# Kernel tuning notes

Hardware: AMD Instinct MI355X
Metric: run time of the kernel (lower is better)

## Reference

```python
import jax, jax.numpy as jnp
import numpy as np

N_NODES = 100000
IN_CH = 128
HID = 16
N_EDGES = 3200000


def setup_inputs() -> dict:
    key = jax.random.key(0)
    k1, k2, k3, k4 = jax.random.split(key, 4)
    x = jax.random.normal(k1, (N_NODES, IN_CH), dtype=jnp.float32)
    edge_index = jax.random.randint(k2, (2, N_EDGES), 0, N_NODES, dtype=jnp.int64)
    s1 = 1.0 / np.sqrt(IN_CH)
    s2 = 1.0 / np.sqrt(HID)
    W1 = jax.random.uniform(k3, (IN_CH, HID), dtype=jnp.float32, minval=-s1, maxval=s1)
    b1 = jnp.zeros((HID,), dtype=jnp.float32)
    W2 = jax.random.uniform(k4, (HID, HID), dtype=jnp.float32, minval=-s2, maxval=s2)
    b2 = jnp.zeros((HID,), dtype=jnp.float32)
    return {"x": x, "edge_index": edge_index, "W1": W1, "b1": b1, "W2": W2, "b2": b2}


def _gcn_layer(h, W, b, row, col, norm, n_nodes):
    # GCNConv: transform first (small hidden dim), then normalized sum aggregation
    h = h @ W  # [N, out]
    msg = h[row] * norm[:, None]  # gather over edges incl. self-loops
    out = jax.ops.segment_sum(msg, col, num_segments=n_nodes)
    return out + b


def reference(x, edge_index, W1, b1, W2, b2):
    n = x.shape[0]
    row, col = edge_index[0], edge_index[1]
    # add self-loops (PyG GCNConv default)
    loop = jnp.arange(n, dtype=edge_index.dtype)
    row_l = jnp.concatenate([row, loop])
    col_l = jnp.concatenate([col, loop])
    # symmetric normalization D^-1/2 (A+I) D^-1/2 (degree from target index)
    deg = jax.ops.segment_sum(jnp.ones_like(col_l, dtype=x.dtype), col_l, num_segments=n)
    dinv = jnp.where(deg > 0, jax.lax.rsqrt(deg), 0.0)
    norm = dinv[row_l] * dinv[col_l]

    h = _gcn_layer(x, W1, b1, row_l, col_l, norm, n)
    h = jax.nn.relu(h)  # dropout is identity at eval
    h = _gcn_layer(h, W2, b2, row_l, col_l, norm, n)

    # fused per-edge dot-product link score + sigmoid (original edges only)
    scores = jnp.sum(h[row] * h[col], axis=-1)
    return jax.nn.sigmoid(scores)
```

## Files before the change

### kernel.cpp

```cpp
#include <hip/hip_runtime.h>
#include <hip/hip_bf16.h>
#include <hip/hip_fp16.h>
#include <math.h>


#define BSH 9
#define BSZ 512
#define CAPB 32768
#define MAXCH 3200
#define MAXCHUNKS 1024

__global__ __launch_bounds__(512) void pSort(
    const int* __restrict__ row, const int* __restrict__ col,
    int* __restrict__ gcur, unsigned int* __restrict__ ebuf,
    int E, int CH, int NBUK) {
    __shared__ unsigned int se[MAXCH];
    __shared__ unsigned short pk[MAXCH];
    __shared__ int lhist[256], lbase[256], lcur[256], gbase[256];
    const int t = threadIdx.x, b = blockIdx.x;
    if (t < 256) lhist[t] = 0;
    __syncthreads();
    const int s = b * CH, e = min(E, s + CH);
    const int cnt = e - s;
    const int n4 = cnt >> 2;
    const int4* c4 = (const int4*)(col + s);
    const int4* r4 = (const int4*)(row + s);
    for (int i = t; i < n4; i += 512) {
        int4 c = c4[i];
        atomicAdd(&lhist[c.x >> BSH], 1);
        atomicAdd(&lhist[c.y >> BSH], 1);
        atomicAdd(&lhist[c.z >> BSH], 1);
        atomicAdd(&lhist[c.w >> BSH], 1);
    }
    for (int i = (n4 << 2) + t; i < cnt; i += 512) atomicAdd(&lhist[col[s + i] >> BSH], 1);
    __syncthreads();
    {
        int own = (t < 256) ? lhist[t] : 0;
        if (t < 256) lcur[t] = own;
        __syncthreads();
        for (int d = 1; d < 256; d <<= 1) {
            int add = (t < 256 && t >= d) ? lcur[t - d] : 0;
            __syncthreads();
            if (t < 256) lcur[t] += add;
            __syncthreads();
        }
        if (t < 256) {
            lbase[t] = lcur[t] - own;
            lcur[t] = lcur[t] - own;
        }
        __syncthreads();
        if (t < NBUK) {
            int base = atomicAdd(&gcur[t], lhist[t]);
            gbase[t] = t * CAPB + base - lbase[t];
        }
    }
    __syncthreads();
    for (int i = t; i < n4; i += 512) {
        int4 c = c4[i];
        int4 r = r4[i];
        int k0 = c.x >> BSH, p0 = atomicAdd(&lcur[k0], 1);
        se[p0] = ((unsigned int)(c.x & (BSZ - 1)) << 17) | (unsigned int)r.x; pk[p0] = (unsigned short)k0;
        int k1 = c.y >> BSH, p1 = atomicAdd(&lcur[k1], 1);
        se[p1] = ((unsigned int)(c.y & (BSZ - 1)) << 17) | (unsigned int)r.y; pk[p1] = (unsigned short)k1;
        int k2 = c.z >> BSH, p2 = atomicAdd(&lcur[k2], 1);
        se[p2] = ((unsigned int)(c.z & (BSZ - 1)) << 17) | (unsigned int)r.z; pk[p2] = (unsigned short)k2;
        int k3 = c.w >> BSH, p3 = atomicAdd(&lcur[k3], 1);
        se[p3] = ((unsigned int)(c.w & (BSZ - 1)) << 17) | (unsigned int)r.w; pk[p3] = (unsigned short)k3;
    }
    for (int i = (n4 << 2) + t; i < cnt; i += 512) {
        int c = col[s + i], r = row[s + i];
        int k = c >> BSH, p = atomicAdd(&lcur[k], 1);
        se[p] = ((unsigned int)(c & (BSZ - 1)) << 17) | (unsigned int)r; pk[p] = (unsigned short)k;
    }
    __syncthreads();
    for (int i = t; i < cnt; i += 512) {
        int k = pk[i];
        ebuf[gbase[k] + i] = se[i];
    }
}

__global__ __launch_bounds__(1024) void pS2G(
    const unsigned int* __restrict__ ebuf, const int* __restrict__ gcur,
    const float* __restrict__ x, const float* __restrict__ W1,
    unsigned int* __restrict__ ebuf2, float* __restrict__ dinv,
    int* __restrict__ start, __half* __restrict__ ts, int N) {
    __shared__ int h[BSZ], sc[BSZ], cur[BSZ];
    __shared__ float wsT[16 * 132];
    const int t = threadIdx.x, k = blockIdx.x;
    if (t < BSZ) h[t] = 0;
    for (int idx = t; idx < 2048; idx += 1024) {
        int kk = idx >> 4, c = idx & 15;
        wsT[c * 132 + kk] = W1[idx];
    }
    __syncthreads();
    const int s = k * CAPB, e = s + gcur[k];
    for (int i = s + t; i < e; i += 1024) atomicAdd(&h[ebuf[i] >> 17], 1);
    __syncthreads();
    if (t < BSZ) sc[t] = h[t];
    __syncthreads();
    for (int d = 1; d < BSZ; d <<= 1) {
        int add = (t < BSZ && t >= d) ? sc[t - d] : 0;
        __syncthreads();
        if (t < BSZ) sc[t] += add;
        __syncthreads();
    }
    if (t < BSZ) {
        cur[t] = sc[t] - h[t];
        const int v = (k << BSH) + t;
        if (v < N) {
            dinv[v] = rsqrtf((float)h[t] + 1.0f);
            start[v] = s + cur[t];
        }
    }
    __syncthreads();
    for (int i = s + t; i < e; i += 1024) {
        unsigned int w = ebuf[i];
        int p = atomicAdd(&cur[w >> 17], 1);
        ebuf2[s + p] = w;
    }
    const int u = t >> 1, half = t & 1;
    const int v = (k << BSH) + u;
    if (v >= N) return;
    const float dv = rsqrtf((float)h[u] + 1.0f);
    const float4* xr = (const float4*)(x + (size_t)v * 128) + half * 16;
    float acc[16];
    #pragma unroll
    for (int c = 0; c < 16; ++c) acc[c] = 0.f;
    const int kbase = half * 16;
    #pragma unroll 8
    for (int k4 = 0; k4 < 16; ++k4) {
        float4 a = xr[k4];
        #pragma unroll
        for (int c = 0; c < 16; ++c) {
            const float4 w = *(const float4*)&wsT[c * 132 + (kbase + k4) * 4];
            acc[c] = fmaf(a.x, w.x, fmaf(a.y, w.y, fmaf(a.z, w.z, fmaf(a.w, w.w, acc[c]))));
        }
    }
    #pragma unroll
    for (int c = 0; c < 16; ++c) acc[c] += __shfl_xor(acc[c], 1);
    union { __half h8[8]; uint4 u4; } o;
    #pragma unroll
    for (int c = 0; c < 8; ++c) o.h8[c] = __float2half(acc[half * 8 + c] * dv);
    ((uint4*)(ts + (size_t)v * 16))[half] = o.u4;
}

__global__ __launch_bounds__(256) void pGat1(
    const unsigned int* __restrict__ ebuf2, const int* __restrict__ start,
    const int* __restrict__ gcur,
    const __half2* __restrict__ tsv, const float* __restrict__ dinv,
    const float* __restrict__ b1, const float* __restrict__ W2,
    __half2* __restrict__ ts2v, int N) {
    __shared__ float w2s[256];
    const int tid = threadIdx.x;
    w2s[tid] = W2[tid];
    __syncthreads();
    const int l = tid & 7;
    const int v = blockIdx.x * 32 + (tid >> 3);
    if (v >= N) return;
    const int s = start[v];
    const int k = v >> BSH;
    const bool lastv = (((v + 1) & (BSZ - 1)) == 0) || (v + 1 >= N);
    const int e = lastv ? (k * CAPB + gcur[k]) : start[v + 1];
    float sx = 0.f, sy = 0.f;
    int i = s;
    for (; i + 8 <= e; i += 8) {
        unsigned int w0 = ebuf2[i],     w1 = ebuf2[i + 1];
        unsigned int w2 = ebuf2[i + 2], w3 = ebuf2[i + 3];
        unsigned int w4 = ebuf2[i + 4], w5 = ebuf2[i + 5];
        unsigned int w6 = ebuf2[i + 6], w7 = ebuf2[i + 7];
        float2 f0 = __half22float2(tsv[(size_t)(w0 & 0x1FFFF) * 8 + l]);
        float2 f1 = __half22float2(tsv[(size_t)(w1 & 0x1FFFF) * 8 + l]);
        float2 f2 = __half22float2(tsv[(size_t)(w2 & 0x1FFFF) * 8 + l]);
        float2 f3 = __half22float2(tsv[(size_t)(w3 & 0x1FFFF) * 8 + l]);
        float2 f4 = __half22float2(tsv[(size_t)(w4 & 0x1FFFF) * 8 + l]);
        float2 f5 = __half22float2(tsv[(size_t)(w5 & 0x1FFFF) * 8 + l]);
        float2 f6 = __half22float2(tsv[(size_t)(w6 & 0x1FFFF) * 8 + l]);
        float2 f7 = __half22float2(tsv[(size_t)(w7 & 0x1FFFF) * 8 + l]);
        sx += ((f0.x + f1.x) + (f2.x + f3.x)) + ((f4.x + f5.x) + (f6.x + f7.x));
        sy += ((f0.y + f1.y) + (f2.y + f3.y)) + ((f4.y + f5.y) + (f6.y + f7.y));
    }
    for (; i + 4 <= e; i += 4) {
        unsigned int w0 = ebuf2[i],     w1 = ebuf2[i + 1];
        unsigned int w2 = ebuf2[i + 2], w3 = ebuf2[i + 3];
        float2 f0 = __half22float2(tsv[(size_t)(w0 & 0x1FFFF) * 8 + l]);
        float2 f1 = __half22float2(tsv[(size_t)(w1 & 0x1FFFF) * 8 + l]);
        float2 f2 = __half22float2(tsv[(size_t)(w2 & 0x1FFFF) * 8 + l]);
        float2 f3 = __half22float2(tsv[(size_t)(w3 & 0x1FFFF) * 8 + l]);
        sx += (f0.x + f1.x) + (f2.x + f3.x);
        sy += (f0.y + f1.y) + (f2.y + f3.y);
    }
    for (; i < e; ++i) {
        unsigned int w = ebuf2[i];
        float2 f = __half22float2(tsv[(size_t)(w & 0x1FFFF) * 8 + l]);
        sx += f.x; sy += f.y;
    }
    const float dv = dinv[v];
    float2 sf = __half22float2(tsv[(size_t)v * 8 + l]);
    float hx = fmaxf(dv * (sx + sf.x) + b1[2 * l],     0.f);
    float hy = fmaxf(dv * (sy + sf.y) + b1[2 * l + 1], 0.f);
    float ox = 0.f, oy = 0.f;
    #pragma unroll
    for (int j = 0; j < 8; ++j) {
        float ax = __shfl(hx, j, 8);
        float ay = __shfl(hy, j, 8);
        ox = fmaf(ax, w2s[(2 * j) * 16 + 2 * l],     fmaf(ay, w2s[(2 * j + 1) * 16 + 2 * l],     ox));
        oy = fmaf(ax, w2s[(2 * j) * 16 + 2 * l + 1], fmaf(ay, w2s[(2 * j + 1) * 16 + 2 * l + 1], oy));
    }
    ts2v[(size_t)v * 8 + l] = __halves2half2(__float2half(dv * ox), __float2half(dv * oy));
}

__global__ __launch_bounds__(256) void pGat2(
    const unsigned int* __restrict__ ebuf2, const int* __restrict__ start,
    const int* __restrict__ gcur,
    const __half2* __restrict__ tsv, const float* __restrict__ dinv,
    const float* __restrict__ b2, __half2* __restrict__ h2v, int N) {
    const int tid = threadIdx.x;
    const int l = tid & 7;
    const int v = blockIdx.x * 32 + (tid >> 3);
    if (v >= N) return;
    const int s = start[v];
    const int k = v >> BSH;
    const bool lastv = (((v + 1) & (BSZ - 1)) == 0) || (v + 1 >= N);
    const int e = lastv ? (k * CAPB + gcur[k]) : start[v + 1];
    float sx = 0.f, sy = 0.f;
    int i = s;
    for (; i + 8 <= e; i += 8) {
        unsigned int w0 = ebuf2[i],     w1 = ebuf2[i + 1];
        unsigned int w2 = ebuf2[i + 2], w3 = ebuf2[i + 3];
        unsigned int w4 = ebuf2[i + 4], w5 = ebuf2[i + 5];
        unsigned int w6 = ebuf2[i + 6], w7 = ebuf2[i + 7];
        float2 f0 = __half22float2(tsv[(size_t)(w0 & 0x1FFFF) * 8 + l]);
        float2 f1 = __half22float2(tsv[(size_t)(w1 & 0x1FFFF) * 8 + l]);
        float2 f2 = __half22float2(tsv[(size_t)(w2 & 0x1FFFF) * 8 + l]);
        float2 f3 = __half22float2(tsv[(size_t)(w3 & 0x1FFFF) * 8 + l]);
        float2 f4 = __half22float2(tsv[(size_t)(w4 & 0x1FFFF) * 8 + l]);
        float2 f5 = __half22float2(tsv[(size_t)(w5 & 0x1FFFF) * 8 + l]);
        float2 f6 = __half22float2(tsv[(size_t)(w6 & 0x1FFFF) * 8 + l]);
        float2 f7 = __half22float2(tsv[(size_t)(w7 & 0x1FFFF) * 8 + l]);
        sx += ((f0.x + f1.x) + (f2.x + f3.x)) + ((f4.x + f5.x) + (f6.x + f7.x));
        sy += ((f0.y + f1.y) + (f2.y + f3.y)) + ((f4.y + f5.y) + (f6.y + f7.y));
    }
    for (; i + 4 <= e; i += 4) {
        unsigned int w0 = ebuf2[i],     w1 = ebuf2[i + 1];
        unsigned int w2 = ebuf2[i + 2], w3 = ebuf2[i + 3];
        float2 f0 = __half22float2(tsv[(size_t)(w0 & 0x1FFFF) * 8 + l]);
        float2 f1 = __half22float2(tsv[(size_t)(w1 & 0x1FFFF) * 8 + l]);
        float2 f2 = __half22float2(tsv[(size_t)(w2 & 0x1FFFF) * 8 + l]);
        float2 f3 = __half22float2(tsv[(size_t)(w3 & 0x1FFFF) * 8 + l]);
        sx += (f0.x + f1.x) + (f2.x + f3.x);
        sy += (f0.y + f1.y) + (f2.y + f3.y);
    }
    for (; i < e; ++i) {
        unsigned int w = ebuf2[i];
        float2 f = __half22float2(tsv[(size_t)(w & 0x1FFFF) * 8 + l]);
        sx += f.x; sy += f.y;
    }
    float2 sf = __half22float2(tsv[(size_t)v * 8 + l]);
    const float dv = dinv[v];
    h2v[(size_t)v * 8 + l] = __halves2half2(
        __float2half(dv * (sx + sf.x) + b2[2 * l]),
        __float2half(dv * (sy + sf.y) + b2[2 * l + 1]));
}

__global__ void k_score(const int* __restrict__ row, const int* __restrict__ col,
                        const __half* __restrict__ h2h, float* __restrict__ out, int E) {
    int e = blockIdx.x * 256 + threadIdx.x;
    if (e < E) {
        union { uint4 u[2]; __half2 h[8]; } a, b;
        const uint4* pa = (const uint4*)(h2h + (size_t)row[e] * 16);
        const uint4* pb = (const uint4*)(h2h + (size_t)col[e] * 16);
        a.u[0] = pa[0]; a.u[1] = pa[1];
        b.u[0] = pb[0]; b.u[1] = pb[1];
        float d = 0.f;
        #pragma unroll
        for (int i = 0; i < 8; ++i) {
            float2 fa = __half22float2(a.h[i]);
            float2 fb = __half22float2(b.h[i]);
            d = fmaf(fa.x, fb.x, fmaf(fa.y, fb.y, d));
        }
        out[e] = 1.0f / (1.0f + __expf(-d));
    }
}

__global__ void k_countf(const int* __restrict__ col, float* __restrict__ deg, int E) {
    int e = blockIdx.x * 256 + threadIdx.x;
    if (e < E) atomicAdd(&deg[col[e]], 1.0f);
}
__global__ void k_dinvf(float* __restrict__ dinv, int N) {
    int v = blockIdx.x * 256 + threadIdx.x;
    if (v < N) dinv[v] = rsqrtf(dinv[v] + 1.0f);
}
__global__ __launch_bounds__(256) void k_gemm1f(
    const float* __restrict__ x, const float* __restrict__ W1,
    const float* __restrict__ dinv, float* __restrict__ ts, int N) {
    __shared__ float wsT[16 * 132];
    const int tid = threadIdx.x;
    for (int idx = tid; idx < 2048; idx += 256) {
        int k = idx >> 4, c = idx & 15;
        wsT[c * 132 + k] = W1[idx];
    }
    __syncthreads();
    const int n = blockIdx.x * 256 + tid;
    if (n >= N) return;
    const float4* xr = (const float4*)(x + (size_t)n * 128);
    float acc[16];
    #pragma unroll
    for (int c = 0; c < 16; ++c) acc[c] = 0.f;
    for (int k4 = 0; k4 < 32; ++k4) {
        float4 a = xr[k4];
        #pragma unroll
        for (int c = 0; c < 16; ++c) {
            const float4 w = *(const float4*)&wsT[c * 132 + k4 * 4];
            acc[c] = fmaf(a.x, w.x, fmaf(a.y, w.y, fmaf(a.z, w.z, fmaf(a.w, w.w, acc[c]))));
        }
    }
    float dv = dinv[n];
    float4* o = (float4*)(ts + (size_t)n * 16);
    #pragma unroll
    for (int q = 0; q < 4; ++q)
        o[q] = make_float4(acc[4*q] * dv, acc[4*q+1] * dv, acc[4*q+2] * dv, acc[4*q+3] * dv);
}
__global__ void k_scatter(const int* __restrict__ row, const int* __restrict__ col,
                          const float* __restrict__ ts, float* __restrict__ acc, int E) {
    int g = blockIdx.x * 256 + threadIdx.x;
    int e = g >> 4, c = g & 15;
    if (e < E) atomicAdd(&acc[(size_t)col[e] * 16 + c], ts[(size_t)row[e] * 16 + c]);
}
__global__ void k_finalize(float* __restrict__ acc, const float* __restrict__ ts,
                           const float* __restrict__ dinv, const float* __restrict__ b,
                           int N, int relu) {
    int g = blockIdx.x * 256 + threadIdx.x;
    int v = g >> 4, c = g & 15;
    if (v < N) {
        float h = dinv[v] * (acc[g] + ts[g]) + b[c];
        if (relu) h = fmaxf(h, 0.f);
        acc[g] = h;
    }
}
__global__ __launch_bounds__(256) void k_gemm2f(
    const float* __restrict__ h1, const float* __restrict__ W2,
    const float* __restrict__ dinv, float* __restrict__ ts2, int N) {
    __shared__ float hs[16 * 17];
    __shared__ float ws2[256];
    const int tid = threadIdx.x;
    const int base = blockIdx.x * 16;
    if (tid < 64) ((float4*)ws2)[tid] = ((const float4*)W2)[tid];
    if (tid >= 64 && tid < 128) {
        int t2 = tid - 64;
        float4 v4 = ((const float4*)(h1 + (size_t)base * 16))[t2];
        float* d = &hs[(t2 >> 2) * 17 + (t2 & 3) * 4];
        d[0] = v4.x; d[1] = v4.y; d[2] = v4.z; d[3] = v4.w;
    }
    __syncthreads();
    const int r = tid >> 4, c = tid & 15;
    float a = 0.f;
    #pragma unroll
    for (int kk = 0; kk < 16; ++kk) a = fmaf(hs[r * 17 + kk], ws2[kk * 16 + c], a);
    ts2[(size_t)(base + r) * 16 + c] = a * dinv[base + r];
}
__global__ void k_scoref(const int* __restrict__ row, const int* __restrict__ col,
                         const float* __restrict__ h2, float* __restrict__ out, int E) {
    int e = blockIdx.x * 256 + threadIdx.x;
    if (e < E) {
        const float4* a = (const float4*)(h2 + (size_t)row[e] * 16);
        const float4* b = (const float4*)(h2 + (size_t)col[e] * 16);
        float d = 0.f;
        #pragma unroll
        for (int i = 0; i < 4; ++i) {
            float4 u = a[i], v = b[i];
            d += u.x * v.x + u.y * v.y + u.z * v.z + u.w * v.w;
        }
        out[e] = 1.0f / (1.0f + __expf(-d));
    }
}

extern "C" void kernel_launch(void* const* d_in, const int* in_sizes, int n_in,
                              void* d_out, int out_size, void* d_ws, size_t ws_size,
                              hipStream_t stream) {
    const float* x  = (const float*)d_in[0];
    const int*   ei = (const int*)d_in[1];
    const float* W1 = (const float*)d_in[2];
    const float* b1 = (const float*)d_in[3];
    const float* W2 = (const float*)d_in[4];
    const float* b2 = (const float*)d_in[5];

    const int N = in_sizes[0] / 128;
    const int E = in_sizes[1] / 2;
    const int* row = ei;
    const int* col = ei + E;
    float* out = (float*)d_out;

    const int NBUK = (N + BSZ - 1) / BSZ;
    const int CN = (E + MAXCH - 1) / MAXCH;
    const int CH = MAXCH;

    char* ws = (char*)d_ws;
    size_t off = 0;
    auto alloc = [&](size_t bytes) { void* p = ws + off; off += (bytes + 255) & ~(size_t)255; return p; };
    float*  dinv  = (float*)alloc((size_t)N * 4);
    __half* ts1h  = (__half*)alloc((size_t)N * 32);
    __half* ts2h  = (__half*)alloc((size_t)N * 32);
    int*    start = (int*)alloc((size_t)(N + 1) * 4);
    int*    gcur  = (int*)alloc((size_t)NBUK * 4);
    unsigned int* ebuf  = (unsigned int*)alloc((size_t)NBUK * CAPB * 4);
    unsigned int* ebuf2 = (unsigned int*)alloc((size_t)NBUK * CAPB * 4);
    const size_t need = off;

    if (N <= 131072 && NBUK <= 256 && CN <= MAXCHUNKS &&
        (size_t)E * 2 <= (size_t)NBUK * CAPB && ws_size >= need) {
        hipMemsetAsync(gcur, 0, (size_t)NBUK * 4, stream);
        pSort<<<CN, 512, 0, stream>>>(row, col, gcur, ebuf, E, CH, NBUK);
        pS2G<<<NBUK, 1024, 0, stream>>>(ebuf, gcur, x, W1, ebuf2, dinv, start, ts1h, N);
        pGat1<<<(N + 31) / 32, 256, 0, stream>>>(ebuf2, start, gcur, (const __half2*)ts1h,
                                                 dinv, b1, W2, (__half2*)ts2h, N);
        __half* h2h = ts1h;
        pGat2<<<(N + 31) / 32, 256, 0, stream>>>(ebuf2, start, gcur, (const __half2*)ts2h,
                                                 dinv, b2, (__half2*)h2h, N);
        k_score<<<(E + 255) / 256, 256, 0, stream>>>(row, col, h2h, out, E);
    } else {
        float* dinvF = (float*)ws;
        float* ts1F  = (float*)(ws + (size_t)N * 4);
        float* ts2F  = (float*)(ws + (size_t)N * 4 + (size_t)N * 64);
        hipMemsetAsync(dinvF, 0, (size_t)N * 4, stream);
        hipMemsetAsync(ts2F, 0, (size_t)N * 64, stream);
        k_countf<<<(E + 255) / 256, 256, 0, stream>>>(col, dinvF, E);
        k_dinvf<<<(N + 255) / 256, 256, 0, stream>>>(dinvF, N);
        k_gemm1f<<<(N + 255) / 256, 256, 0, stream>>>(x, W1, dinvF, ts1F, N);
        k_scatter<<<(E * 16) / 256, 256, 0, stream>>>(row, col, ts1F, ts2F, E);
        k_finalize<<<(N * 16 + 255) / 256, 256, 0, stream>>>(ts2F, ts1F, dinvF, b1, N, 1);
        k_gemm2f<<<N / 16, 256, 0, stream>>>(ts2F, W2, dinvF, ts1F, N);
        hipMemsetAsync(ts2F, 0, (size_t)N * 64, stream);
        k_scatter<<<(E * 16) / 256, 256, 0, stream>>>(row, col, ts1F, ts2F, E);
        k_finalize<<<(N * 16 + 255) / 256, 256, 0, stream>>>(ts2F, ts1F, dinvF, b2, N, 0);
        k_scoref<<<(E + 255) / 256, 256, 0, stream>>>(row, col, ts2F, out, E);
    }
}
```

Before: 258.9 us.

## Shrink node buckets to 128, widen sort histogram, cache bucket edges in registers

Buckets now hold 128 destination nodes instead of 512, giving 782 buckets, so the pS2G per-bucket kernel launches about four times as many blocks (512 threads each) and fills more compute units. pSort uses 1024 threads and 1024-entry local histograms to match the larger bucket count. pS2G keeps each thread's bucket edges in registers (up to 12 per thread) between the counting pass and the scatter pass, avoiding a second global read of ebuf. The x·W1 transform is split over 4 lanes per node. The trade-offs are more bucket atomics and global-cursor contention in pSort, a longer prefix scan, and extra register pressure.

```diff
diff --git a/kernel.cpp b/kernel.cpp
--- a/kernel.cpp
+++ b/kernel.cpp
@@ -4,50 +4,49 @@
 #include <math.h>
 
 
-#define BSH 9
-#define BSZ 512
-#define CAPB 32768
+#define BSH 7
+#define BSZ 128
+#define CAPB 8192
+#define RCAP 12
 #define MAXCH 3200
 #define MAXCHUNKS 1024
 
-__global__ __launch_bounds__(512) void pSort(
+__global__ __launch_bounds__(1024) void pSort(
     const int* __restrict__ row, const int* __restrict__ col,
     int* __restrict__ gcur, unsigned int* __restrict__ ebuf,
     int E, int CH, int NBUK) {
     __shared__ unsigned int se[MAXCH];
     __shared__ unsigned short pk[MAXCH];
-    __shared__ int lhist[256], lbase[256], lcur[256], gbase[256];
+    __shared__ int lhist[1024], lbase[1024], lcur[1024], gbase[1024];
     const int t = threadIdx.x, b = blockIdx.x;
-    if (t < 256) lhist[t] = 0;
+    lhist[t] = 0;
     __syncthreads();
     const int s = b * CH, e = min(E, s + CH);
     const int cnt = e - s;
     const int n4 = cnt >> 2;
     const int4* c4 = (const int4*)(col + s);
     const int4* r4 = (const int4*)(row + s);
-    for (int i = t; i < n4; i += 512) {
+    for (int i = t; i < n4; i += 1024) {
         int4 c = c4[i];
         atomicAdd(&lhist[c.x >> BSH], 1);
         atomicAdd(&lhist[c.y >> BSH], 1);
         atomicAdd(&lhist[c.z >> BSH], 1);
         atomicAdd(&lhist[c.w >> BSH], 1);
     }
-    for (int i = (n4 << 2) + t; i < cnt; i += 512) atomicAdd(&lhist[col[s + i] >> BSH], 1);
+    for (int i = (n4 << 2) + t; i < cnt; i += 1024) atomicAdd(&lhist[col[s + i] >> BSH], 1);
     __syncthreads();
     {
-        int own = (t < 256) ? lhist[t] : 0;
-        if (t < 256) lcur[t] = own;
+        int own = lhist[t];
+        lcur[t] = own;
         __syncthreads();
-        for (int d = 1; d < 256; d <<= 1) {
-            int add = (t < 256 && t >= d) ? lcur[t - d] : 0;
+        for (int d = 1; d < 1024; d <<= 1) {
+            int add = (t >= d) ? lcur[t - d] : 0;
             __syncthreads();
-            if (t < 256) lcur[t] += add;
+            lcur[t] += add;
             __syncthreads();
         }
-        if (t < 256) {
-            lbase[t] = lcur[t] - own;
-            lcur[t] = lcur[t] - own;
-        }
+        lbase[t] = lcur[t] - own;
+        lcur[t] = lbase[t];
         __syncthreads();
         if (t < NBUK) {
             int base = atomicAdd(&gcur[t], lhist[t]);
@@ -55,7 +54,7 @@
         }
     }
     __syncthreads();
-    for (int i = t; i < n4; i += 512) {
+    for (int i = t; i < n4; i += 1024) {
         int4 c = c4[i];
         int4 r = r4[i];
         int k0 = c.x >> BSH, p0 = atomicAdd(&lcur[k0], 1);
@@ -67,19 +66,19 @@
         int k3 = c.w >> BSH, p3 = atomicAdd(&lcur[k3], 1);
         se[p3] = ((unsigned int)(c.w & (BSZ - 1)) << 17) | (unsigned int)r.w; pk[p3] = (unsigned short)k3;
     }
-    for (int i = (n4 << 2) + t; i < cnt; i += 512) {
+    for (int i = (n4 << 2) + t; i < cnt; i += 1024) {
         int c = col[s + i], r = row[s + i];
         int k = c >> BSH, p = atomicAdd(&lcur[k], 1);
         se[p] = ((unsigned int)(c & (BSZ - 1)) << 17) | (unsigned int)r; pk[p] = (unsigned short)k;
     }
     __syncthreads();
-    for (int i = t; i < cnt; i += 512) {
+    for (int i = t; i < cnt; i += 1024) {
         int k = pk[i];
         ebuf[gbase[k] + i] = se[i];
     }
 }
 
-__global__ __launch_bounds__(1024) void pS2G(
+__global__ __launch_bounds__(512) void pS2G(
     const unsigned int* __restrict__ ebuf, const int* __restrict__ gcur,
     const float* __restrict__ x, const float* __restrict__ W1,
     unsigned int* __restrict__ ebuf2, float* __restrict__ dinv,
@@ -88,13 +87,25 @@
     __shared__ float wsT[16 * 132];
     const int t = threadIdx.x, k = blockIdx.x;
     if (t < BSZ) h[t] = 0;
-    for (int idx = t; idx < 2048; idx += 1024) {
+    for (int idx = t; idx < 2048; idx += 512) {
         int kk = idx >> 4, c = idx & 15;
         wsT[c * 132 + kk] = W1[idx];
     }
     __syncthreads();
     const int s = k * CAPB, e = s + gcur[k];
-    for (int i = s + t; i < e; i += 1024) atomicAdd(&h[ebuf[i] >> 17], 1);
+    const int cnt = e - s;
+    unsigned int r[RCAP];
+    const bool fits = (cnt <= 512 * RCAP);
+    if (fits) {
+        int nr = 0;
+        for (int i = s + t; i < e; i += 512) {
+            unsigned int w = ebuf[i];
+            r[nr++] = w;
+            atomicAdd(&h[w >> 17], 1);
+        }
+    } else {
+        for (int i = s + t; i < e; i += 512) atomicAdd(&h[ebuf[i] >> 17], 1);
+    }
     __syncthreads();
     if (t < BSZ) sc[t] = h[t];
     __syncthreads();
@@ -113,35 +124,47 @@
         }
     }
     __syncthreads();
-    for (int i = s + t; i < e; i += 1024) {
-        unsigned int w = ebuf[i];
-        int p = atomicAdd(&cur[w >> 17], 1);
-        ebuf2[s + p] = w;
-    }
-    const int u = t >> 1, half = t & 1;
+    if (fits) {
+        int nr = 0;
+        for (int i = s + t; i < e; i += 512) {
+            unsigned int w = r[nr++];
+            int p = atomicAdd(&cur[w >> 17], 1);
+            ebuf2[s + p] = w;
+        }
+    } else {
+        for (int i = s + t; i < e; i += 512) {
+            unsigned int w = ebuf[i];
+            int p = atomicAdd(&cur[w >> 17], 1);
+            ebuf2[s + p] = w;
+        }
+    }
+    const int u = t >> 2, q = t & 3;
     const int v = (k << BSH) + u;
     if (v >= N) return;
     const float dv = rsqrtf((float)h[u] + 1.0f);
-    const float4* xr = (const float4*)(x + (size_t)v * 128) + half * 16;
+    const float4* xr = (const float4*)(x + (size_t)v * 128);
     float acc[16];
     #pragma unroll
     for (int c = 0; c < 16; ++c) acc[c] = 0.f;
-    const int kbase = half * 16;
-    #pragma unroll 8
-    for (int k4 = 0; k4 < 16; ++k4) {
-        float4 a = xr[k4];
+    #pragma unroll
+    for (int k4 = 0; k4 < 8; ++k4) {
+        const int kk = q + 4 * k4;
+        float4 a = xr[kk];
         #pragma unroll
         for (int c = 0; c < 16; ++c) {
-            const float4 w = *(const float4*)&wsT[c * 132 + (kbase + k4) * 4];
+            const float4 w = *(const float4*)&wsT[c * 132 + kk * 4];
             acc[c] = fmaf(a.x, w.x, fmaf(a.y, w.y, fmaf(a.z, w.z, fmaf(a.w, w.w, acc[c]))));
         }
     }
     #pragma unroll
-    for (int c = 0; c < 16; ++c) acc[c] += __shfl_xor(acc[c], 1);
-    union { __half h8[8]; uint4 u4; } o;
-    #pragma unroll
-    for (int c = 0; c < 8; ++c) o.h8[c] = __float2half(acc[half * 8 + c] * dv);
-    ((uint4*)(ts + (size_t)v * 16))[half] = o.u4;
+    for (int c = 0; c < 16; ++c) {
+        acc[c] += __shfl_xor(acc[c], 1);
+        acc[c] += __shfl_xor(acc[c], 2);
+    }
+    union { __half h4[4]; uint2 u2; } o;
+    #pragma unroll
+    for (int c = 0; c < 4; ++c) o.h4[c] = __float2half(acc[q * 4 + c] * dv);
+    ((uint2*)(ts + (size_t)v * 16))[q] = o.u2;
 }
 
 __global__ __launch_bounds__(256) void pGat1(
@@ -406,11 +429,11 @@
     unsigned int* ebuf2 = (unsigned int*)alloc((size_t)NBUK * CAPB * 4);
     const size_t need = off;
 
-    if (N <= 131072 && NBUK <= 256 && CN <= MAXCHUNKS &&
+    if (N <= 131072 && NBUK <= 1024 && CN <= MAXCHUNKS &&
         (size_t)E * 2 <= (size_t)NBUK * CAPB && ws_size >= need) {
         hipMemsetAsync(gcur, 0, (size_t)NBUK * 4, stream);
-        pSort<<<CN, 512, 0, stream>>>(row, col, gcur, ebuf, E, CH, NBUK);
-        pS2G<<<NBUK, 1024, 0, stream>>>(ebuf, gcur, x, W1, ebuf2, dinv, start, ts1h, N);
+        pSort<<<CN, 1024, 0, stream>>>(row, col, gcur, ebuf, E, CH, NBUK);
+        pS2G<<<NBUK, 512, 0, stream>>>(ebuf, gcur, x, W1, ebuf2, dinv, start, ts1h, N);
         pGat1<<<(N + 31) / 32, 256, 0, stream>>>(ebuf2, start, gcur, (const __half2*)ts1h,
                                                  dinv, b1, W2, (__half2*)ts2h, N);
         __half* h2h = ts1h;
```

Result: no change. 256.6 us (-0.9%).
